# Optimization experiments

Hardware: AMD Instinct MI355X
Metric: run time of the kernel (lower is better)

## Reference

```python
import jax, jax.numpy as jnp
import numpy as np

DIM = 768
NUM_HEADS = 12
SMALLEST_RATIO = 0.25
LARGEST_RATIO = 1.0


def setup_inputs() -> dict:
    key = jax.random.key(0)
    k0, k1, k2 = jax.random.split(key, 3)
    B, N = 4, 2048
    x = jax.random.normal(k0, (B, N, DIM), dtype=jnp.float32)
    Wqkv = jax.random.normal(k1, (3 * DIM, DIM), dtype=jnp.float32) * 0.02
    bqkv = jnp.zeros((3 * DIM,), dtype=jnp.float32)
    Wproj = jax.random.normal(k2, (DIM, DIM), dtype=jnp.float32) * 0.02
    bproj = jnp.zeros((DIM,), dtype=jnp.float32)
    return {"x": x, "Wqkv": Wqkv, "bqkv": bqkv, "Wproj": Wproj, "bproj": bproj, "ratio": 1}


def reference(x, Wqkv, bqkv, Wproj, bproj, ratio):
    dc = int(ratio * DIM)
    # dynamic slimmable-width slicing: smallest/largest ratio take leading block,
    # intermediate ratios take trailing block
    if ratio == SMALLEST_RATIO or ratio == LARGEST_RATIO:
        wq, bq = Wqkv[: dc * 3, :dc], bqkv[: dc * 3]
        wp, bp = Wproj[:dc, :dc], bproj[:dc]
    else:
        wq, bq = Wqkv[-dc * 3 :, -dc:], bqkv[-dc * 3 :]
        wp, bp = Wproj[-dc:, -dc:], bproj[-dc:]
    B, N, C = x.shape
    hd = C // NUM_HEADS
    scale = (DIM // NUM_HEADS) ** -0.5  # set at init from full dim, not sliced C
    qkv = x @ wq.T + bq                               # [B, N, 3C]
    qkv = qkv.reshape(B, N, 3, NUM_HEADS, hd).transpose(2, 0, 3, 1, 4)  # [3,B,H,N,hd]
    q, k, v = qkv[0], qkv[1], qkv[2]
    attn = jax.nn.softmax(jnp.einsum("bhqd,bhkd->bhqk", q, k) * scale, axis=-1)
    out = jnp.einsum("bhqk,bhkd->bhqd", attn, v)      # [B,H,N,hd]
    out = out.transpose(0, 2, 1, 3).reshape(B, N, C)
    return out @ wp.T + bp
```

## Files before the change

### kernel.cpp

```cpp
#include <hip/hip_runtime.h>

typedef __bf16 bf16x8 __attribute__((ext_vector_type(8)));
typedef __bf16 bf16x2 __attribute__((ext_vector_type(2)));
typedef float  f32x4  __attribute__((ext_vector_type(4)));
typedef float  f32x16 __attribute__((ext_vector_type(16)));
typedef unsigned short u16;
typedef unsigned u32x2 __attribute__((ext_vector_type(2)));
typedef unsigned u32x4 __attribute__((ext_vector_type(4)));

__device__ __forceinline__ u16 f2bf(float f) {
  return __builtin_bit_cast(u16, (__bf16)f);
}
__device__ __forceinline__ unsigned pack2(float lo, float hi) {
  bf16x2 t;
  t[0] = (__bf16)lo; t[1] = (__bf16)hi;
  return __builtin_bit_cast(unsigned, t);
}

#define GLOAD16(g, l) __builtin_amdgcn_global_load_lds( \
    (__attribute__((address_space(1))) void*)(void*)(g), \
    (__attribute__((address_space(3))) void*)(l), 16, 0, 0)

#define QSCALE 0.18033688011112042f

__global__ __launch_bounds__(256) void cvt_bf16(const float* __restrict__ src,
                                                unsigned* __restrict__ dst, int n8) {
  int i = blockIdx.x * 256 + threadIdx.x;
  if (i >= n8) return;
  const float4* s = (const float4*)src + 2 * (size_t)i;
  float4 a = s[0], b = s[1];
  u32x4 o = {pack2(a.x, a.y), pack2(a.z, a.w), pack2(b.x, b.y), pack2(b.z, b.w)};
  *((u32x4*)dst + i) = o;
}

template<int EPI>
__global__ __launch_bounds__(256) void gemm_tn(
    const u16* __restrict__ A, const u16* __restrict__ B,
    const float* __restrict__ bias, float* __restrict__ outF,
    u16* __restrict__ qws, u16* __restrict__ kws, u16* __restrict__ vtws,
    int M, int N, int K) {
  __shared__ __align__(16) u16 As[8192];
  __shared__ __align__(16) u16 Bs[8192];
  const int tid = threadIdx.x;
  const int ln = tid & 63, wv = tid >> 6;
  const int wr = wv >> 1, wc = wv & 1;
  const int m0 = blockIdx.x * 128, n0 = blockIdx.y * 128;

  f32x4 acc[4][4] = {};

  const int c0 = tid, c1 = tid + 256;
  const int r0 = c0 >> 2, kc0 = ((c0 & 3) ^ ((r0 >> 1) & 3)) * 8;
  const int r1 = c1 >> 2, kc1 = ((c1 & 3) ^ ((r1 >> 1) & 3)) * 8;
  const u16* ag0 = A + (size_t)(m0 + r0) * K + kc0;
  const u16* ag1 = A + (size_t)(m0 + r1) * K + kc1;
  const u16* bg0 = B + (size_t)(n0 + r0) * K + kc0;
  const u16* bg1 = B + (size_t)(n0 + r1) * K + kc1;

  GLOAD16(ag0, As + wv * 512);
  GLOAD16(ag1, As + 2048 + wv * 512);
  GLOAD16(bg0, Bs + wv * 512);
  GLOAD16(bg1, Bs + 2048 + wv * 512);
  __syncthreads();

  int cur = 0;
  for (int k0 = 0; k0 < K; k0 += 32) {
    const int nxt = cur ^ 1;
    if (k0 + 32 < K) {
      GLOAD16(ag0 + k0 + 32, As + nxt * 4096 + wv * 512);
      GLOAD16(ag1 + k0 + 32, As + nxt * 4096 + 2048 + wv * 512);
      GLOAD16(bg0 + k0 + 32, Bs + nxt * 4096 + wv * 512);
      GLOAD16(bg1 + k0 + 32, Bs + nxt * 4096 + 2048 + wv * 512);
    }
    const u16* ab = As + cur * 4096;
    const u16* bb = Bs + cur * 4096;
    bf16x8 af[4], bfr[4];
#pragma unroll
    for (int i = 0; i < 4; ++i) {
      int ra = wr * 64 + i * 16 + (ln & 15);
      af[i] = *(const bf16x8*)(ab + ra * 32 + (((ln >> 4) ^ ((ra >> 1) & 3)) * 8));
      int rb = wc * 64 + i * 16 + (ln & 15);
      bfr[i] = *(const bf16x8*)(bb + rb * 32 + (((ln >> 4) ^ ((rb >> 1) & 3)) * 8));
    }
#pragma unroll
    for (int i = 0; i < 4; ++i)
#pragma unroll
      for (int j = 0; j < 4; ++j)
        acc[i][j] = __builtin_amdgcn_mfma_f32_16x16x32_bf16(af[i], bfr[j], acc[i][j], 0, 0, 0);
    __syncthreads();
    cur = nxt;
  }

  if (EPI == 1) {
#pragma unroll
    for (int j = 0; j < 4; ++j) {
      int col = n0 + wc * 64 + j * 16 + (ln & 15);
      float bj = bias[col];
#pragma unroll
      for (int i = 0; i < 4; ++i) {
        int mr = m0 + wr * 64 + i * 16 + ((ln >> 4) << 2);
#pragma unroll
        for (int r = 0; r < 4; ++r)
          outF[(size_t)(mr + r) * N + col] = acc[i][j][r] + bj;
      }
    }
  } else {
    const int s = n0 / 768;
#pragma unroll
    for (int j = 0; j < 4; ++j) {
      int col = n0 + wc * 64 + j * 16 + (ln & 15);
      float bj = bias[col];
      int ns = col - s * 768;
      int h = ns >> 6, d = ns & 63;
#pragma unroll
      for (int i = 0; i < 4; ++i) {
        int m = m0 + wr * 64 + i * 16 + ((ln >> 4) << 2);
        int b = m >> 11, iseq = m & 2047;
        size_t bh = (size_t)(b * 12 + h);
        if (s == 0) {
#pragma unroll
          for (int r = 0; r < 4; ++r)
            qws[(bh * 2048 + iseq + r) * 64 + d] = f2bf((acc[i][j][r] + bj) * QSCALE);
        } else if (s == 1) {
#pragma unroll
          for (int r = 0; r < 4; ++r)
            kws[(bh * 2048 + iseq + r) * 64 + d] = f2bf(acc[i][j][r] + bj);
        } else {
          u32x2 pk = {pack2(acc[i][j][0] + bj, acc[i][j][1] + bj),
                      pack2(acc[i][j][2] + bj, acc[i][j][3] + bj)};
          *(u32x2*)(vtws + ((size_t)bh * 64 + (iseq >> 5)) * 2048 +
                    ((iseq >> 3) & 3) * 512 + (size_t)d * 8 + (iseq & 7)) = pk;
        }
      }
    }
  }
}

#define SWZ(v) (((v) & 32) | (((v) & 31) ^ (ln & 31)))
__global__ __launch_bounds__(256, 3) void attn_fa(
    const u16* __restrict__ qws, const u16* __restrict__ kws,
    const u16* __restrict__ vtws, u16* __restrict__ aows) {
  __shared__ __align__(16) u16 SM[16384];
  __shared__ float Ls[256];
  const int tid = threadIdx.x, ln = tid & 63, wv = tid >> 6;
  const int lq = ln & 31, hi = ln >> 5;
  const int qw = wv & 1;
  const int p  = wv >> 1;

  const int flat = blockIdx.y * 16 + blockIdx.x;
  const int xcd = flat & 7, jj = flat >> 3;
  const int bh = xcd * 6 + (jj % 6);
  const int q0 = (jj / 6) * 128 + qw * 64;

  const int kv0 = p * 1024;
  const size_t kbase = (size_t)bh * 2048 * 64;

  bf16x8 qf[2][4];
#pragma unroll
  for (int g = 0; g < 2; ++g) {
    const u16* qp = qws + kbase + (size_t)(q0 + g * 32 + lq) * 64 + hi * 8;
#pragma unroll
    for (int dc = 0; dc < 4; ++dc) qf[g][dc] = *(const bf16x8*)(qp + dc * 16);
  }

  const f32x16 zc = {};
  f32x16 o0[2] = {}, o1[2] = {};
  float lsum[2] = {0.f, 0.f};

  int koff[4], voff[2];
#pragma unroll
  for (int dc = 0; dc < 4; ++dc)
    koff[dc] = lq * 64 + (((dc * 2 + hi) ^ (lq & 7)) * 8);
#pragma unroll
  for (int c = 0; c < 2; ++c)
    voff[c] = (c * 2 + hi) * 512 + lq * 8;

  const int s0i = qw * 128 + ln, s1i = s0i + 64;
  const int kvA = s0i >> 3, kvB = s1i >> 3;
  const int piA = (kvA & ~12) | ((kvA & 4) << 1) | ((kvA & 8) >> 1);
  const int piB = (kvB & ~12) | ((kvB & 4) << 1) | ((kvB & 8) >> 1);
  const u16* kg0 = kws + kbase + (size_t)(kv0 + piA) * 64 + (((s0i & 7) ^ (kvA & 7)) * 8);
  const u16* kg1 = kws + kbase + (size_t)(kv0 + piB) * 64 + (((s1i & 7) ^ (kvB & 7)) * 8);
  const u16* vg  = vtws + ((size_t)bh * 64 + (kv0 >> 5)) * 2048 + s0i * 8;
  u16* Kb = SM + p * 4096;
  u16* Vb = SM + 8192 + p * 4096;
  const int sd = qw * 1024;

#define STAGE(buf, kb, t) do { \
    GLOAD16(kg0 + (size_t)(kb) * 64, Kb + (buf) * 2048 + sd); \
    GLOAD16(kg1 + (size_t)(kb) * 64, Kb + (buf) * 2048 + sd + 512); \
    GLOAD16(vg + (size_t)(t) * 2048, Vb + (buf) * 2048 + sd); \
    GLOAD16(vg + (size_t)(t) * 2048 + 512, Vb + (buf) * 2048 + sd + 512); \
  } while (0)

  STAGE(0, 0, 0);
  __syncthreads();

  int cur = 0;
  for (int it = 0; it < 32; ++it) {
    const int nxt = cur ^ 1;
    if (it + 1 < 32) STAGE(nxt, (it + 1) * 32, it + 1);
    const u16* kbuf = Kb + cur * 2048;
    const u16* vbuf = Vb + cur * 2048;

    f32x16 s[2];
    {
      bf16x8 kf = *(const bf16x8*)(kbuf + koff[0]);
      s[0] = __builtin_amdgcn_mfma_f32_32x32x16_bf16(kf, qf[0][0], zc, 0, 0, 0);
      s[1] = __builtin_amdgcn_mfma_f32_32x32x16_bf16(kf, qf[1][0], zc, 0, 0, 0);
    }
#pragma unroll
    for (int dc = 1; dc < 4; ++dc) {
      bf16x8 kf = *(const bf16x8*)(kbuf + koff[dc]);
      s[0] = __builtin_amdgcn_mfma_f32_32x32x16_bf16(kf, qf[0][dc], s[0], 0, 0, 0);
      s[1] = __builtin_amdgcn_mfma_f32_32x32x16_bf16(kf, qf[1][dc], s[1], 0, 0, 0);
    }

#pragma unroll
    for (int g = 0; g < 2; ++g) {
      float a = 0.f;
#pragma unroll
      for (int r = 0; r < 16; ++r) {
        float e = __builtin_amdgcn_exp2f(s[g][r]); s[g][r] = e; a += e;
      }
      lsum[g] += a;
    }

#pragma unroll
    for (int c = 0; c < 2; ++c) {
      bf16x8 va = *(const bf16x8*)(vbuf + voff[c]);
      bf16x8 vb2 = *(const bf16x8*)(vbuf + voff[c] + 256);
#pragma unroll
      for (int g = 0; g < 2; ++g) {
        const int base = c * 8;
        u32x4 pw = {pack2(s[g][base + 0], s[g][base + 1]),
                    pack2(s[g][base + 2], s[g][base + 3]),
                    pack2(s[g][base + 4], s[g][base + 5]),
                    pack2(s[g][base + 6], s[g][base + 7])};
        bf16x8 pfrag = __builtin_bit_cast(bf16x8, pw);
        o0[g] = __builtin_amdgcn_mfma_f32_32x32x16_bf16(va, pfrag, o0[g], 0, 0, 0);
        o1[g] = __builtin_amdgcn_mfma_f32_32x32x16_bf16(vb2, pfrag, o1[g], 0, 0, 0);
      }
    }
    __syncthreads();
    cur = nxt;
  }
#undef STAGE

  float lg[2];
#pragma unroll
  for (int g = 0; g < 2; ++g) {
    lg[g] = lsum[g];
    lg[g] += __shfl_xor(lg[g], 32);
  }

  float* exO = (float*)SM + qw * 4096 + ln * 64;
  if (p == 1) {
#pragma unroll
    for (int r = 0; r < 16; ++r) {
      exO[SWZ(r)]      = o0[0][r];
      exO[SWZ(16 + r)] = o1[0][r];
      exO[SWZ(32 + r)] = o0[1][r];
      exO[SWZ(48 + r)] = o1[1][r];
    }
    Ls[qw * 128 + ln * 2 + 0] = lg[0];
    Ls[qw * 128 + ln * 2 + 1] = lg[1];
  }
  __syncthreads();
  if (p == 0) {
#pragma unroll
    for (int r = 0; r < 16; ++r) {
      o0[0][r] += exO[SWZ(r)];
      o1[0][r] += exO[SWZ(16 + r)];
      o0[1][r] += exO[SWZ(32 + r)];
      o1[1][r] += exO[SWZ(48 + r)];
    }
    lg[0] += Ls[qw * 128 + ln * 2 + 0];
    lg[1] += Ls[qw * 128 + ln * 2 + 1];

    const int b = bh / 12, h = bh % 12;
#pragma unroll
    for (int g = 0; g < 2; ++g) {
      const float rl = 1.0f / lg[g];
      u16* orow = aows + (size_t)(b * 2048 + q0 + g * 32 + lq) * 768 + h * 64;
#pragma unroll
      for (int t = 0; t < 4; ++t) {
        u32x2 pk0 = {pack2(o0[g][4 * t + 0] * rl, o0[g][4 * t + 1] * rl),
                     pack2(o0[g][4 * t + 2] * rl, o0[g][4 * t + 3] * rl)};
        u32x2 pk1 = {pack2(o1[g][4 * t + 0] * rl, o1[g][4 * t + 1] * rl),
                     pack2(o1[g][4 * t + 2] * rl, o1[g][4 * t + 3] * rl)};
        *(u32x2*)(orow + t * 8 + 4 * hi)      = pk0;
        *(u32x2*)(orow + 32 + t * 8 + 4 * hi) = pk1;
      }
    }
  }
}

extern "C" void kernel_launch(void* const* d_in, const int* in_sizes, int n_in,
                              void* d_out, int out_size, void* d_ws, size_t ws_size,
                              hipStream_t stream) {
  const float* x     = (const float*)d_in[0];
  const float* Wqkv  = (const float*)d_in[1];
  const float* bqkv  = (const float*)d_in[2];
  const float* Wproj = (const float*)d_in[3];
  const float* bproj = (const float*)d_in[4];
  float* out = (float*)d_out;

  u16* xb   = (u16*)d_ws;
  u16* wqb  = xb  + 6291456;
  u16* wpb  = wqb + 1769472;
  u16* qws  = wpb + 589824;
  u16* kws  = qws + 6291456;
  u16* vtws = kws + 6291456;
  u16* aows = vtws + 6291456;

  cvt_bf16<<<6291456 / 8 / 256, 256, 0, stream>>>(x, (unsigned*)xb, 6291456 / 8);
  cvt_bf16<<<1769472 / 8 / 256, 256, 0, stream>>>(Wqkv, (unsigned*)wqb, 1769472 / 8);
  cvt_bf16<<<589824 / 8 / 256, 256, 0, stream>>>(Wproj, (unsigned*)wpb, 589824 / 8);

  gemm_tn<0><<<dim3(64, 18), 256, 0, stream>>>(xb, wqb, bqkv, nullptr,
                                               qws, kws, vtws, 8192, 2304, 768);
  attn_fa<<<dim3(16, 48), 256, 0, stream>>>(qws, kws, vtws, aows);
  gemm_tn<1><<<dim3(64, 6), 256, 0, stream>>>(aows, wpb, bproj, out,
                                              nullptr, nullptr, nullptr,
                                              8192, 768, 768);
}
```

Before: 139.1 us.

## Triple-buffer K/V staging with single barrier per iteration and MFMA priority

```diff
diff --git a/kernel.cpp b/kernel.cpp
--- a/kernel.cpp
+++ b/kernel.cpp
@@ -139,7 +139,7 @@
 __global__ __launch_bounds__(256, 3) void attn_fa(
     const u16* __restrict__ qws, const u16* __restrict__ kws,
     const u16* __restrict__ vtws, u16* __restrict__ aows) {
-  __shared__ __align__(16) u16 SM[16384];
+  __shared__ __align__(16) u16 SM[24576];
   __shared__ float Ls[256];
   const int tid = threadIdx.x, ln = tid & 63, wv = tid >> 6;
   const int lq = ln & 31, hi = ln >> 5;
@@ -181,28 +181,36 @@
   const u16* kg0 = kws + kbase + (size_t)(kv0 + piA) * 64 + (((s0i & 7) ^ (kvA & 7)) * 8);
   const u16* kg1 = kws + kbase + (size_t)(kv0 + piB) * 64 + (((s1i & 7) ^ (kvB & 7)) * 8);
   const u16* vg  = vtws + ((size_t)bh * 64 + (kv0 >> 5)) * 2048 + s0i * 8;
-  u16* Kb = SM + p * 4096;
-  u16* Vb = SM + 8192 + p * 4096;
+  u16* Kb = SM + p * 6144;
+  u16* Vb = SM + 12288 + p * 6144;
   const int sd = qw * 1024;
 
-#define STAGE(buf, kb, t) do { \
-    GLOAD16(kg0 + (size_t)(kb) * 64, Kb + (buf) * 2048 + sd); \
-    GLOAD16(kg1 + (size_t)(kb) * 64, Kb + (buf) * 2048 + sd + 512); \
+#define STAGE(buf, t) do { \
+    GLOAD16(kg0 + (size_t)(t) * 2048, Kb + (buf) * 2048 + sd); \
+    GLOAD16(kg1 + (size_t)(t) * 2048, Kb + (buf) * 2048 + sd + 512); \
     GLOAD16(vg + (size_t)(t) * 2048, Vb + (buf) * 2048 + sd); \
     GLOAD16(vg + (size_t)(t) * 2048 + 512, Vb + (buf) * 2048 + sd + 512); \
   } while (0)
 
-  STAGE(0, 0, 0);
-  __syncthreads();
+  STAGE(0, 0);
+  STAGE(1, 1);
 
   int cur = 0;
   for (int it = 0; it < 32; ++it) {
-    const int nxt = cur ^ 1;
-    if (it + 1 < 32) STAGE(nxt, (it + 1) * 32, it + 1);
+    if (it < 31) {
+      asm volatile("s_waitcnt vmcnt(4)\n\ts_barrier" ::: "memory");
+    } else {
+      asm volatile("s_waitcnt vmcnt(0)\n\ts_barrier" ::: "memory");
+    }
+    if (it + 2 < 32) {
+      const int sb = (cur + 2 >= 3) ? cur - 1 : cur + 2;
+      STAGE(sb, it + 2);
+    }
     const u16* kbuf = Kb + cur * 2048;
     const u16* vbuf = Vb + cur * 2048;
 
     f32x16 s[2];
+    __builtin_amdgcn_s_setprio(1);
     {
       bf16x8 kf = *(const bf16x8*)(kbuf + koff[0]);
       s[0] = __builtin_amdgcn_mfma_f32_32x32x16_bf16(kf, qf[0][0], zc, 0, 0, 0);
@@ -214,17 +222,20 @@
       s[0] = __builtin_amdgcn_mfma_f32_32x32x16_bf16(kf, qf[0][dc], s[0], 0, 0, 0);
       s[1] = __builtin_amdgcn_mfma_f32_32x32x16_bf16(kf, qf[1][dc], s[1], 0, 0, 0);
     }
+    __builtin_amdgcn_s_setprio(0);
 
 #pragma unroll
     for (int g = 0; g < 2; ++g) {
-      float a = 0.f;
-#pragma unroll
-      for (int r = 0; r < 16; ++r) {
-        float e = __builtin_amdgcn_exp2f(s[g][r]); s[g][r] = e; a += e;
-      }
-      lsum[g] += a;
-    }
-
+      float a = 0.f, b2 = 0.f;
+#pragma unroll
+      for (int r = 0; r < 16; r += 2) {
+        float e0 = __builtin_amdgcn_exp2f(s[g][r]);     s[g][r] = e0;     a  += e0;
+        float e1 = __builtin_amdgcn_exp2f(s[g][r + 1]); s[g][r + 1] = e1; b2 += e1;
+      }
+      lsum[g] += a + b2;
+    }
+
+    __builtin_amdgcn_s_setprio(1);
 #pragma unroll
     for (int c = 0; c < 2; ++c) {
       bf16x8 va = *(const bf16x8*)(vbuf + voff[c]);
@@ -241,10 +252,12 @@
         o1[g] = __builtin_amdgcn_mfma_f32_32x32x16_bf16(vb2, pfrag, o1[g], 0, 0, 0);
       }
     }
-    __syncthreads();
-    cur = nxt;
+    __builtin_amdgcn_s_setprio(0);
+    cur = (cur + 1 == 3) ? 0 : cur + 1;
   }
 #undef STAGE
+
+  __syncthreads();
 
   float lg[2];
 #pragma unroll
```

After: 140.5 us. No clear change (+1.0%).
